# Kernel tuning notes

Measured on AMD Instinct MI355X. Metric: run time of the kernel, lower is better.

## Reference

```python
import jax, jax.numpy as jnp
import numpy as np

N_NODES = 100000   # n_nodes
N_EDGES = 1600000  # n_nodes * avg_degree(16)
D_IN = 128
D_OUT = 128


def setup_inputs() -> dict:
    key = jax.random.key(0)
    k1, k2, k3, k4, k5 = jax.random.split(key, 5)
    h = jax.random.normal(k1, (N_NODES, D_IN), dtype=jnp.float32)
    edge_src = jax.random.randint(k2, (N_EDGES,), 0, N_NODES, dtype=jnp.int32)
    edge_dst = jax.random.randint(k3, (N_EDGES,), 0, N_NODES, dtype=jnp.int32)
    # Linear params, init per reset_parameters: U(-stdv, stdv), stdv = 1/sqrt(in_feats)
    stdv = 1.0 / np.sqrt(D_IN)
    W = jax.random.uniform(k4, (D_OUT, D_IN), dtype=jnp.float32, minval=-stdv, maxval=stdv)
    b = jax.random.uniform(k5, (D_OUT,), dtype=jnp.float32, minval=-stdv, maxval=stdv)
    return {"h": h, "edge_src": edge_src, "edge_dst": edge_dst, "W": W, "b": b}


def reference(h, edge_src, edge_dst, W, b):
    # update_all(copy_src('h'), sum) == neighbor-sum aggregation (SpMM with 0/1 adjacency)
    ah = jax.ops.segment_sum(h[edge_src], edge_dst, num_segments=N_NODES)  # [N, D_IN]
    # dense linear + activation fused on the aggregated features
    return jax.nn.relu(ah @ W.T + b)  # [N, D_OUT]
```

## Files before the change

kernel.cpp:

```cpp
#include <hip/hip_runtime.h>

#define D 128
#define BKT_SHIFT 9
#define BKT_SIZE 512
#define P1_EPB 4096
#define CNT_BLOCKS 256
#define PARTIALS_INTS (256 * 256)
#define SW_LDU 68

typedef __attribute__((ext_vector_type(8))) short bf16x8;
typedef __attribute__((ext_vector_type(4))) float f32x4;

__device__ inline unsigned int pack2bf(float a, float b) {
    unsigned int ua = __float_as_uint(a);
    unsigned int ub = __float_as_uint(b);
    ua = (ua + 0x7fffu + ((ua >> 16) & 1u)) >> 16;
    ub = (ub + 0x7fffu + ((ub >> 16) & 1u)) >> 16;
    return ua | (ub << 16);
}
__device__ inline unsigned short pack1bf(float a) {
    unsigned int ua = __float_as_uint(a);
    return (unsigned short)((ua + 0x7fffu + ((ua >> 16) & 1u)) >> 16);
}


__global__ __launch_bounds__(256) void bucket_count_kernel(
    const int* __restrict__ edst, int* __restrict__ partials, int n_edges, int epb)
{
    __shared__ int hcnt[256];
    const int tid = threadIdx.x;
    hcnt[tid] = 0;
    __syncthreads();
    const int base = blockIdx.x * epb;
    const int lim = min(epb, n_edges - base);
    int k = tid;
    for (; k + 768 < lim; k += 1024) {
        int d0 = edst[base + k];
        int d1 = edst[base + k + 256];
        int d2 = edst[base + k + 512];
        int d3 = edst[base + k + 768];
        atomicAdd(&hcnt[d0 >> BKT_SHIFT], 1);
        atomicAdd(&hcnt[d1 >> BKT_SHIFT], 1);
        atomicAdd(&hcnt[d2 >> BKT_SHIFT], 1);
        atomicAdd(&hcnt[d3 >> BKT_SHIFT], 1);
    }
    for (; k < lim; k += 256)
        atomicAdd(&hcnt[edst[base + k] >> BKT_SHIFT], 1);
    __syncthreads();
    partials[(blockIdx.x << 8) + tid] = hcnt[tid];
}

__global__ __launch_bounds__(256) void bucket_scan_kernel(
    const int* __restrict__ partials, int* __restrict__ bucketBase,
    int* __restrict__ bucketCur, int nbk)
{
    __shared__ int s[256];
    const int t = threadIdx.x;
    int sum = 0;
    #pragma unroll 8
    for (int b = 0; b < CNT_BLOCKS; b++) sum += partials[(b << 8) + t];
    int v = (t < nbk) ? sum : 0;
    s[t] = v;
    __syncthreads();
    #pragma unroll
    for (int off = 1; off < 256; off <<= 1) {
        int x = (t >= off) ? s[t - off] : 0;
        __syncthreads();
        s[t] += x;
        __syncthreads();
    }
    if (t < nbk) {
        int base = s[t] - v;
        bucketBase[t] = base;
        bucketCur[t] = base;
    }
}

__global__ __launch_bounds__(256) void p1_partition_kernel(
    const int* __restrict__ esrc, const int* __restrict__ edst,
    int* __restrict__ bucketCur, unsigned int* __restrict__ pairs, int n_edges)
{
    __shared__ int hist[256];
    __shared__ int lbase[256];
    __shared__ int gbase[256];
    __shared__ int cur[256];
    __shared__ unsigned int buf[P1_EPB];
    __shared__ unsigned char bkt8[P1_EPB];
    const int tid = threadIdx.x;
    const int base = blockIdx.x * P1_EPB;
    hist[tid] = 0;
    __syncthreads();
    unsigned int pk[16]; int bk[16];
    #pragma unroll
    for (int k = 0; k < 16; k++) {
        int e = base + k * 256 + tid;
        if (e < n_edges) {
            int sv = esrc[e], dv = edst[e];
            bk[k] = dv >> BKT_SHIFT;
            pk[k] = ((unsigned)sv << BKT_SHIFT) | (unsigned)(dv & (BKT_SIZE - 1));
            atomicAdd(&hist[bk[k]], 1);
        } else bk[k] = -1;
    }
    __syncthreads();
    const int v = hist[tid];
    if (v > 0) gbase[tid] = atomicAdd(&bucketCur[tid], v);
    lbase[tid] = v;
    __syncthreads();
    #pragma unroll
    for (int off = 1; off < 256; off <<= 1) {
        int x = (tid >= off) ? lbase[tid - off] : 0;
        __syncthreads();
        lbase[tid] += x;
        __syncthreads();
    }
    const int excl = lbase[tid] - v;
    __syncthreads();
    lbase[tid] = excl;
    cur[tid] = excl;
    __syncthreads();
    #pragma unroll
    for (int k = 0; k < 16; k++) {
        if (bk[k] >= 0) {
            int loc = atomicAdd(&cur[bk[k]], 1);
            buf[loc] = pk[k];
            bkt8[loc] = (unsigned char)bk[k];
        }
    }
    __syncthreads();
    const int total = min(P1_EPB, n_edges - base);
    for (int i = tid; i < total; i += 256) {
        int b = bkt8[i];
        pairs[gbase[b] + (i - lbase[b])] = buf[i];
    }
}

__global__ __launch_bounds__(256) void p2_sort_gemm_kernel(
    const unsigned int* __restrict__ pairs, const int* __restrict__ bucketBase,
    int* __restrict__ sorted_src, int* __restrict__ gstart, int* __restrict__ gend,
    const float* __restrict__ h, const float* __restrict__ W,
    unsigned short* __restrict__ z,
    int n_nodes, int n_edges, int nbk)
{
    __shared__ union SU {
        struct { int hist[BKT_SIZE]; int cur[BKT_SIZE]; int sb[256]; } s;
        unsigned int sW[128 * SW_LDU];
    } u;
    const int tid = threadIdx.x;

    if ((int)blockIdx.x < nbk) {
        const int bkt = blockIdx.x;
        const int nbase = bkt << BKT_SHIFT;
        const int pstart = bucketBase[bkt];
        const int pend = (bkt == nbk - 1) ? n_edges : bucketBase[bkt + 1];
        u.s.hist[tid] = 0; u.s.hist[tid + 256] = 0;
        __syncthreads();
        {
            int j = pstart + tid;
            for (; j + 768 < pend; j += 1024) {
                unsigned int q0 = pairs[j];
                unsigned int q1 = pairs[j + 256];
                unsigned int q2 = pairs[j + 512];
                unsigned int q3 = pairs[j + 768];
                atomicAdd(&u.s.hist[q0 & (BKT_SIZE - 1)], 1);
                atomicAdd(&u.s.hist[q1 & (BKT_SIZE - 1)], 1);
                atomicAdd(&u.s.hist[q2 & (BKT_SIZE - 1)], 1);
                atomicAdd(&u.s.hist[q3 & (BKT_SIZE - 1)], 1);
            }
            for (; j < pend; j += 256)
                atomicAdd(&u.s.hist[pairs[j] & (BKT_SIZE - 1)], 1);
        }
        __syncthreads();
        int a  = u.s.hist[2 * tid];
        int b2 = u.s.hist[2 * tid + 1];
        int psum = a + b2;
        u.s.sb[tid] = psum;
        __syncthreads();
        #pragma unroll
        for (int off = 1; off < 256; off <<= 1) {
            int x = (tid >= off) ? u.s.sb[tid - off] : 0;
            __syncthreads();
            u.s.sb[tid] += x;
            __syncthreads();
        }
        int pexcl = u.s.sb[tid] - psum;
        u.s.cur[2 * tid] = pexcl;
        u.s.cur[2 * tid + 1] = pexcl + a;
        __syncthreads();
        for (int i = tid; i < BKT_SIZE; i += 256) {
            int nd = nbase + i;
            if (nd < n_nodes) {
                int st = pstart + u.s.cur[i];
                gstart[nd] = st;
                gend[nd] = st + u.s.hist[i];
            }
        }
        __syncthreads();
        {
            int j = pstart + tid;
            for (; j + 768 < pend; j += 1024) {
                unsigned int q0 = pairs[j];
                unsigned int q1 = pairs[j + 256];
                unsigned int q2 = pairs[j + 512];
                unsigned int q3 = pairs[j + 768];
                int p0 = pstart + atomicAdd(&u.s.cur[q0 & (BKT_SIZE - 1)], 1);
                int p1 = pstart + atomicAdd(&u.s.cur[q1 & (BKT_SIZE - 1)], 1);
                int p2 = pstart + atomicAdd(&u.s.cur[q2 & (BKT_SIZE - 1)], 1);
                int p3 = pstart + atomicAdd(&u.s.cur[q3 & (BKT_SIZE - 1)], 1);
                sorted_src[p0] = (int)(q0 >> BKT_SHIFT);
                sorted_src[p1] = (int)(q1 >> BKT_SHIFT);
                sorted_src[p2] = (int)(q2 >> BKT_SHIFT);
                sorted_src[p3] = (int)(q3 >> BKT_SHIFT);
            }
            for (; j < pend; j += 256) {
                unsigned int p = pairs[j];
                int local = p & (BKT_SIZE - 1);
                int pos = pstart + atomicAdd(&u.s.cur[local], 1);
                sorted_src[pos] = (int)(p >> BKT_SHIFT);
            }
        }
    } else {
        const int gbid = blockIdx.x - nbk;
        for (int i = tid; i < 4096; i += 256) {
            float4 w = ((const float4*)W)[i];
            int row = i >> 5, c4 = i & 31;
            unsigned int* dst = &u.sW[row * SW_LDU + c4 * 2];
            dst[0] = pack2bf(w.x, w.y);
            dst[1] = pack2bf(w.z, w.w);
        }
        __syncthreads();

        const int wave = tid >> 6;
        const int lane = tid & 63;
        const int m = lane & 15;
        const int q = lane >> 4;
        const int r0 = gbid * 64 + wave * 16;
        const int arow = r0 + m;
        const bool rvalid = arow < n_nodes;

        bf16x8 afrag[4];
        #pragma unroll
        for (int ks = 0; ks < 4; ks++) {
            float4 x = make_float4(0.f, 0.f, 0.f, 0.f), y = x;
            if (rvalid) {
                const float4* p = (const float4*)(h + (size_t)arow * D + ks * 32 + q * 8);
                x = p[0]; y = p[1];
            }
            union { unsigned int uu[4]; bf16x8 v; } cvt;
            cvt.uu[0] = pack2bf(x.x, x.y);
            cvt.uu[1] = pack2bf(x.z, x.w);
            cvt.uu[2] = pack2bf(y.x, y.y);
            cvt.uu[3] = pack2bf(y.z, y.w);
            afrag[ks] = cvt.v;
        }

        f32x4 acc[8];
        #pragma unroll
        for (int ct = 0; ct < 8; ct++) acc[ct] = (f32x4){0.f, 0.f, 0.f, 0.f};

        #pragma unroll
        for (int ct = 0; ct < 8; ct++) {
            #pragma unroll
            for (int ks = 0; ks < 4; ks++) {
                const unsigned int* p = &u.sW[(ct * 16 + m) * SW_LDU + ks * 16 + q * 4];
                union { uint4 uu; bf16x8 v; } bu;
                bu.uu = *(const uint4*)p;
                acc[ct] = __builtin_amdgcn_mfma_f32_16x16x32_bf16(afrag[ks], bu.v, acc[ct], 0, 0, 0);
            }
        }

        __syncthreads();
        unsigned short* lds_us = (unsigned short*)u.sW;
        #pragma unroll
        for (int ct = 0; ct < 8; ct++) {
            #pragma unroll
            for (int i = 0; i < 4; i++) {
                lds_us[(wave * 16 + q * 4 + i) * 130 + ct * 16 + m] = pack1bf(acc[ct][i]);
            }
        }
        __syncthreads();
        const unsigned int* lds32 = (const unsigned int*)u.sW;
        const int r0blk = gbid * 64;
        #pragma unroll
        for (int pass = 0; pass < 4; pass++) {
            int idx = pass * 256 + tid;
            int row = idx >> 4;
            int c16 = idx & 15;
            int r = r0blk + row;
            if (r < n_nodes) {
                int bo = row * 65 + c16 * 4;
                uint4 val;
                val.x = lds32[bo]; val.y = lds32[bo + 1];
                val.z = lds32[bo + 2]; val.w = lds32[bo + 3];
                ((uint4*)z)[(size_t)r * 16 + c16] = val;
            }
        }
    }
}

__global__ __launch_bounds__(256) void p2_sort_kernel(
    const unsigned int* __restrict__ pairs, const int* __restrict__ bucketBase,
    int* __restrict__ sorted_src, int* __restrict__ gstart, int* __restrict__ gend,
    int n_nodes, int n_edges, int nbk)
{
    __shared__ int hist[BKT_SIZE];
    __shared__ int cur[BKT_SIZE];
    __shared__ int sb[256];
    const int tid = threadIdx.x;
    const int bkt = blockIdx.x;
    const int nbase = bkt << BKT_SHIFT;
    const int pstart = bucketBase[bkt];
    const int pend = (bkt == nbk - 1) ? n_edges : bucketBase[bkt + 1];
    hist[tid] = 0; hist[tid + 256] = 0;
    __syncthreads();
    for (int j = pstart + tid; j < pend; j += 256)
        atomicAdd(&hist[pairs[j] & (BKT_SIZE - 1)], 1);
    __syncthreads();
    int a  = hist[2 * tid];
    int b2 = hist[2 * tid + 1];
    int psum = a + b2;
    sb[tid] = psum;
    __syncthreads();
    #pragma unroll
    for (int off = 1; off < 256; off <<= 1) {
        int x = (tid >= off) ? sb[tid - off] : 0;
        __syncthreads();
        sb[tid] += x;
        __syncthreads();
    }
    int pexcl = sb[tid] - psum;
    cur[2 * tid] = pexcl;
    cur[2 * tid + 1] = pexcl + a;
    __syncthreads();
    for (int i = tid; i < BKT_SIZE; i += 256) {
        int nd = nbase + i;
        if (nd < n_nodes) {
            int st = pstart + cur[i];
            gstart[nd] = st;
            gend[nd] = st + hist[i];
        }
    }
    __syncthreads();
    for (int j = pstart + tid; j < pend; j += 256) {
        unsigned int p = pairs[j];
        int local = p & (BKT_SIZE - 1);
        int pos = pstart + atomicAdd(&cur[local], 1);
        sorted_src[pos] = (int)(p >> BKT_SHIFT);
    }
}

__global__ __launch_bounds__(256) void gemm_z_kernel(
    const float* __restrict__ h, const float* __restrict__ W,
    unsigned short* __restrict__ z, int n_nodes)
{
    __shared__ unsigned int sW[128 * SW_LDU];
    const int tid = threadIdx.x;
    for (int i = tid; i < 4096; i += 256) {
        float4 w = ((const float4*)W)[i];
        int row = i >> 5, c4 = i & 31;
        unsigned int* dst = &sW[row * SW_LDU + c4 * 2];
        dst[0] = pack2bf(w.x, w.y);
        dst[1] = pack2bf(w.z, w.w);
    }
    __syncthreads();

    const int wave = tid >> 6;
    const int lane = tid & 63;
    const int m = lane & 15;
    const int q = lane >> 4;
    const int r0 = blockIdx.x * 64 + wave * 16;
    const int arow = r0 + m;
    const bool rvalid = arow < n_nodes;

    bf16x8 afrag[4];
    #pragma unroll
    for (int ks = 0; ks < 4; ks++) {
        float4 x = make_float4(0.f, 0.f, 0.f, 0.f), y = x;
        if (rvalid) {
            const float4* p = (const float4*)(h + (size_t)arow * D + ks * 32 + q * 8);
            x = p[0]; y = p[1];
        }
        union { unsigned int u[4]; bf16x8 v; } cvt;
        cvt.u[0] = pack2bf(x.x, x.y);
        cvt.u[1] = pack2bf(x.z, x.w);
        cvt.u[2] = pack2bf(y.x, y.y);
        cvt.u[3] = pack2bf(y.z, y.w);
        afrag[ks] = cvt.v;
    }

    f32x4 acc[8];
    #pragma unroll
    for (int ct = 0; ct < 8; ct++) acc[ct] = (f32x4){0.f, 0.f, 0.f, 0.f};

    #pragma unroll
    for (int ct = 0; ct < 8; ct++) {
        #pragma unroll
        for (int ks = 0; ks < 4; ks++) {
            const unsigned int* p = &sW[(ct * 16 + m) * SW_LDU + ks * 16 + q * 4];
            union { uint4 u; bf16x8 v; } bu;
            bu.u = *(const uint4*)p;
            acc[ct] = __builtin_amdgcn_mfma_f32_16x16x32_bf16(afrag[ks], bu.v, acc[ct], 0, 0, 0);
        }
    }

    __syncthreads();
    unsigned short* lds_us = (unsigned short*)sW;
    #pragma unroll
    for (int ct = 0; ct < 8; ct++) {
        #pragma unroll
        for (int i = 0; i < 4; i++) {
            lds_us[(wave * 16 + q * 4 + i) * 130 + ct * 16 + m] = pack1bf(acc[ct][i]);
        }
    }
    __syncthreads();
    const unsigned int* lds32 = (const unsigned int*)sW;
    const int r0blk = blockIdx.x * 64;
    #pragma unroll
    for (int pass = 0; pass < 4; pass++) {
        int idx = pass * 256 + tid;
        int row = idx >> 4;
        int c16 = idx & 15;
        int r = r0blk + row;
        if (r < n_nodes) {
            int bo = row * 65 + c16 * 4;
            uint4 val;
            val.x = lds32[bo]; val.y = lds32[bo + 1];
            val.z = lds32[bo + 2]; val.w = lds32[bo + 3];
            ((uint4*)z)[(size_t)r * 16 + c16] = val;
        }
    }
}

__global__ __launch_bounds__(256) void gather_row_kernel(
    const unsigned short* __restrict__ z, const int* __restrict__ gstart,
    const int* __restrict__ gend, const int* __restrict__ sorted_src,
    const float* __restrict__ b, float* __restrict__ out, int n_nodes,
    int node_base)
{
    const int tid = threadIdx.x;
    const int node = node_base + blockIdx.x * 16 + (tid >> 4);
    const int lane = tid & 15;
    if (node >= n_nodes) return;
    int e = gstart[node];
    const int end = gend[node];
    const uint4* __restrict__ z4 = (const uint4*)z;
    float acc[8];
    #pragma unroll
    for (int i = 0; i < 8; i++) acc[i] = 0.f;
#define ADDV(v) do { \
    acc[0] += __uint_as_float((v).x << 16); acc[1] += __uint_as_float((v).x & 0xffff0000u); \
    acc[2] += __uint_as_float((v).y << 16); acc[3] += __uint_as_float((v).y & 0xffff0000u); \
    acc[4] += __uint_as_float((v).z << 16); acc[5] += __uint_as_float((v).z & 0xffff0000u); \
    acc[6] += __uint_as_float((v).w << 16); acc[7] += __uint_as_float((v).w & 0xffff0000u); } while (0)
    for (; e + 4 <= end; e += 4) {
        int s0 = sorted_src[e + 0];
        int s1 = sorted_src[e + 1];
        int s2 = sorted_src[e + 2];
        int s3 = sorted_src[e + 3];
        uint4 v0 = z4[(size_t)s0 * 16 + lane];
        uint4 v1 = z4[(size_t)s1 * 16 + lane];
        uint4 v2 = z4[(size_t)s2 * 16 + lane];
        uint4 v3 = z4[(size_t)s3 * 16 + lane];
        ADDV(v0); ADDV(v1); ADDV(v2); ADDV(v3);
    }
    for (; e < end; e++) {
        uint4 v = z4[(size_t)sorted_src[e] * 16 + lane];
        ADDV(v);
    }
#undef ADDV
    float4 b0 = ((const float4*)b)[lane * 2];
    float4 b1 = ((const float4*)b)[lane * 2 + 1];
    float4* o = (float4*)(out + (size_t)node * D + lane * 8);
    o[0] = make_float4(fmaxf(acc[0] + b0.x, 0.f), fmaxf(acc[1] + b0.y, 0.f),
                       fmaxf(acc[2] + b0.z, 0.f), fmaxf(acc[3] + b0.w, 0.f));
    o[1] = make_float4(fmaxf(acc[4] + b1.x, 0.f), fmaxf(acc[5] + b1.y, 0.f),
                       fmaxf(acc[6] + b1.z, 0.f), fmaxf(acc[7] + b1.w, 0.f));
}


__global__ __launch_bounds__(256) void hist_kernel(
    const int* __restrict__ edst, int* __restrict__ cnt, int n_edges)
{
    int gid = blockIdx.x * 256 + threadIdx.x;
    if (gid < n_edges) atomicAdd(&cnt[edst[gid]], 1);
}

__global__ __launch_bounds__(256) void scanA_kernel(
    const int* __restrict__ cnt, int* __restrict__ localoff,
    int* __restrict__ blocksums, int n)
{
    __shared__ int s[256];
    const int t = threadIdx.x;
    const int base = blockIdx.x * 1024 + t * 4;
    int v[4]; int sum = 0;
    #pragma unroll
    for (int i = 0; i < 4; i++) {
        int idx = base + i;
        v[i] = (idx < n) ? cnt[idx] : 0;
        sum += v[i];
    }
    s[t] = sum;
    __syncthreads();
    #pragma unroll
    for (int off = 1; off < 256; off <<= 1) {
        int x = (t >= off) ? s[t - off] : 0;
        __syncthreads();
        s[t] += x;
        __syncthreads();
    }
    int excl = s[t] - sum;
    int run = 0;
    #pragma unroll
    for (int i = 0; i < 4; i++) {
        int idx = base + i;
        if (idx < n) localoff[idx] = excl + run;
        run += v[i];
    }
    if (t == 255) blocksums[blockIdx.x] = s[255];
}

__global__ __launch_bounds__(256) void scanB_kernel(
    const int* __restrict__ blocksums, int* __restrict__ blockoffs, int nb)
{
    __shared__ int s[256];
    const int t = threadIdx.x;
    int v = (t < nb) ? blocksums[t] : 0;
    s[t] = v;
    __syncthreads();
    #pragma unroll
    for (int off = 1; off < 256; off <<= 1) {
        int x = (t >= off) ? s[t - off] : 0;
        __syncthreads();
        s[t] += x;
        __syncthreads();
    }
    if (t < nb) blockoffs[t] = s[t] - v;
}

__global__ __launch_bounds__(256) void scanC_kernel(
    const int* __restrict__ localoff, const int* __restrict__ blockoffs,
    int* __restrict__ outoffs, int* __restrict__ cursor, int n)
{
    int gid = blockIdx.x * 256 + threadIdx.x;
    if (gid >= n) return;
    int v = localoff[gid] + blockoffs[blockIdx.x >> 2];
    outoffs[gid] = v;
    if (cursor) cursor[gid] = v;
}

__global__ __launch_bounds__(256) void place_kernel(
    const int* __restrict__ esrc, const int* __restrict__ edst,
    int* __restrict__ cursor, int* __restrict__ sorted_src, int n_edges)
{
    int gid = blockIdx.x * 256 + threadIdx.x;
    if (gid >= n_edges) return;
    int d = edst[gid];
    int pos = atomicAdd(&cursor[d], 1);
    sorted_src[pos] = esrc[gid];
}

__global__ __launch_bounds__(256) void gather_kernel(
    const float* __restrict__ h, const int* __restrict__ offs,
    const int* __restrict__ endp, const int* __restrict__ sorted_src,
    float* __restrict__ out, int n_nodes)
{
    const int tid = threadIdx.x;
    const int node = blockIdx.x * 8 + (tid >> 5);
    const int lane = tid & 31;
    if (node >= n_nodes) return;
    const int start = offs[node];
    const int end = endp[node];
    const float4* __restrict__ h4 = (const float4*)h;
    float4 acc = make_float4(0.f, 0.f, 0.f, 0.f);
    for (int e = start; e < end; e++) {
        float4 a = h4[(size_t)sorted_src[e] * 32 + lane];
        acc.x += a.x; acc.y += a.y; acc.z += a.z; acc.w += a.w;
    }
    ((float4*)out)[(size_t)node * 32 + lane] = acc;
}

__global__ __launch_bounds__(256) void scatter_kernel(
    const float* __restrict__ h, const int* __restrict__ esrc,
    const int* __restrict__ edst, float* __restrict__ out, int n_edges)
{
    int gid = blockIdx.x * 256 + threadIdx.x;
    int e = gid >> 5;
    int l = gid & 31;
    if (e >= n_edges) return;
    int s = esrc[e];
    int d = edst[e];
    float4 v = ((const float4*)(h + (size_t)s * D))[l];
    float* o = out + (size_t)d * D + (size_t)l * 4;
    atomicAdd(o + 0, v.x);
    atomicAdd(o + 1, v.y);
    atomicAdd(o + 2, v.z);
    atomicAdd(o + 3, v.w);
}

__global__ __launch_bounds__(256) void mfma_gemm_relu_kernel(
    float* __restrict__ io, const float* __restrict__ W,
    const float* __restrict__ b, int n_nodes)
{
    __shared__ unsigned int sW[128 * SW_LDU];
    const int tid = threadIdx.x;
    for (int i = tid; i < 4096; i += 256) {
        float4 w = ((const float4*)W)[i];
        int row = i >> 5, c4 = i & 31;
        unsigned int* dst = &sW[row * SW_LDU + c4 * 2];
        dst[0] = pack2bf(w.x, w.y);
        dst[1] = pack2bf(w.z, w.w);
    }
    __syncthreads();
    const int wave = tid >> 6;
    const int lane = tid & 63;
    const int m = lane & 15;
    const int q = lane >> 4;
    const int r0 = blockIdx.x * 64 + wave * 16;
    const int arow = r0 + m;
    const bool rvalid = arow < n_nodes;
    bf16x8 afrag[4];
    #pragma unroll
    for (int ks = 0; ks < 4; ks++) {
        float4 x = make_float4(0.f, 0.f, 0.f, 0.f), y = x;
        if (rvalid) {
            const float4* p = (const float4*)(io + (size_t)arow * D + ks * 32 + q * 8);
            x = p[0]; y = p[1];
        }
        union { unsigned int u[4]; bf16x8 v; } cvt;
        cvt.u[0] = pack2bf(x.x, x.y);
        cvt.u[1] = pack2bf(x.z, x.w);
        cvt.u[2] = pack2bf(y.x, y.y);
        cvt.u[3] = pack2bf(y.z, y.w);
        afrag[ks] = cvt.v;
    }
    f32x4 acc[8];
    #pragma unroll
    for (int ct = 0; ct < 8; ct++) acc[ct] = (f32x4){0.f, 0.f, 0.f, 0.f};
    #pragma unroll
    for (int ct = 0; ct < 8; ct++) {
        #pragma unroll
        for (int ks = 0; ks < 4; ks++) {
            const unsigned int* p = &sW[(ct * 16 + m) * SW_LDU + ks * 16 + q * 4];
            union { uint4 u; bf16x8 v; } bu;
            bu.u = *(const uint4*)p;
            acc[ct] = __builtin_amdgcn_mfma_f32_16x16x32_bf16(afrag[ks], bu.v, acc[ct], 0, 0, 0);
        }
    }
    #pragma unroll
    for (int ct = 0; ct < 8; ct++) {
        int col = ct * 16 + m;
        float bias = b[col];
        #pragma unroll
        for (int i = 0; i < 4; i++) {
            int r = r0 + q * 4 + i;
            if (r < n_nodes) {
                float v = acc[ct][i] + bias;
                io[(size_t)r * D + col] = v > 0.f ? v : 0.f;
            }
        }
    }
}

extern "C" void kernel_launch(void* const* d_in, const int* in_sizes, int n_in,
                              void* d_out, int out_size, void* d_ws, size_t ws_size,
                              hipStream_t stream) {
    const float* h    = (const float*)d_in[0];
    const int*   esrc = (const int*)d_in[1];
    const int*   edst = (const int*)d_in[2];
    const float* W    = (const float*)d_in[3];
    const float* b    = (const float*)d_in[4];
    float* out = (float*)d_out;
    const int n_nodes = in_sizes[0] / D;
    const int n_edges = in_sizes[1];
    const int NB  = (n_nodes + 1023) / 1024;
    const int NBK = (n_nodes + BKT_SIZE - 1) / BKT_SIZE;

    size_t fixed = ((size_t)2 * n_nodes + PARTIALS_INTS + 2 * NBK + (size_t)n_edges) * 4;
    size_t pairs_off = (fixed + 15) & ~(size_t)15;
    size_t z_off = (pairs_off + (size_t)n_edges * 4 + 15) & ~(size_t)15;
    size_t need_fused = z_off + (size_t)n_nodes * D * 2;

    size_t zone_bytes = (size_t)n_edges * 4;
    size_t zb2 = (size_t)n_nodes * D * 2;
    if (zb2 > zone_bytes) zone_bytes = zb2;
    size_t need_main = pairs_off + zone_bytes;

    const int cnt_epb = (n_edges + CNT_BLOCKS - 1) / CNT_BLOCKS;

    if (ws_size >= need_fused && NBK <= 256 && n_nodes <= (1 << 22)) {
        int* gstart     = (int*)d_ws;
        int* gend       = gstart + n_nodes;
        int* partials   = gend + n_nodes;
        int* bucketBase = partials + PARTIALS_INTS;
        int* bucketCur  = bucketBase + NBK;
        int* sorted_src = bucketCur + NBK;
        unsigned int* pairs = (unsigned int*)((char*)d_ws + pairs_off);
        unsigned short* z   = (unsigned short*)((char*)d_ws + z_off);

        bucket_count_kernel<<<CNT_BLOCKS, 256, 0, stream>>>(
            edst, partials, n_edges, cnt_epb);
        bucket_scan_kernel<<<1, 256, 0, stream>>>(partials, bucketBase, bucketCur, NBK);
        p1_partition_kernel<<<(n_edges + P1_EPB - 1) / P1_EPB, 256, 0, stream>>>(
            esrc, edst, bucketCur, pairs, n_edges);
        const int gemmBlocks = (n_nodes + 63) / 64;
        p2_sort_gemm_kernel<<<NBK + gemmBlocks, 256, 0, stream>>>(
            pairs, bucketBase, sorted_src, gstart, gend, h, W, z,
            n_nodes, n_edges, NBK);
        gather_row_kernel<<<(n_nodes + 15) / 16, 256, 0, stream>>>(
            z, gstart, gend, sorted_src, b, out, n_nodes, 0);
        return;
    }

    if (ws_size >= need_main && NBK <= 256 && n_nodes <= (1 << 23)) {
        int* gstart     = (int*)d_ws;
        int* gend       = gstart + n_nodes;
        int* partials   = gend + n_nodes;
        int* bucketBase = partials + PARTIALS_INTS;
        int* bucketCur  = bucketBase + NBK;
        int* sorted_src = bucketCur + NBK;
        void* zone = (char*)d_ws + pairs_off;
        unsigned int* pairs = (unsigned int*)zone;
        unsigned short* z = (unsigned short*)zone;

        bucket_count_kernel<<<CNT_BLOCKS, 256, 0, stream>>>(
            edst, partials, n_edges, cnt_epb);
        bucket_scan_kernel<<<1, 256, 0, stream>>>(partials, bucketBase, bucketCur, NBK);
        p1_partition_kernel<<<(n_edges + P1_EPB - 1) / P1_EPB, 256, 0, stream>>>(
            esrc, edst, bucketCur, pairs, n_edges);
        p2_sort_kernel<<<NBK, 256, 0, stream>>>(
            pairs, bucketBase, sorted_src, gstart, gend, n_nodes, n_edges, NBK);
        gemm_z_kernel<<<(n_nodes + 63) / 64, 256, 0, stream>>>(h, W, z, n_nodes);
        gather_row_kernel<<<(n_nodes + 15) / 16, 256, 0, stream>>>(
            z, gstart, gend, sorted_src, b, out, n_nodes, 0);
        return;
    }

    size_t csr_ints = (size_t)3 * n_nodes + 2 * NB + (size_t)n_edges;
    size_t needB = csr_ints * sizeof(int);
    if (ws_size >= needB && NB <= 256) {
        int* cnt        = (int*)d_ws;
        int* offs       = cnt + n_nodes;
        int* cursor     = offs + n_nodes;
        int* blocksums  = cursor + n_nodes;
        int* blockoffs  = blocksums + NB;
        int* sorted_src = blockoffs + NB;

        hipMemsetAsync(cnt, 0, (size_t)n_nodes * sizeof(int), stream);
        hist_kernel<<<(n_edges + 255) / 256, 256, 0, stream>>>(edst, cnt, n_edges);
        scanA_kernel<<<NB, 256, 0, stream>>>(cnt, offs, blocksums, n_nodes);
        scanB_kernel<<<1, 256, 0, stream>>>(blocksums, blockoffs, NB);
        scanC_kernel<<<(n_nodes + 255) / 256, 256, 0, stream>>>(
            offs, blockoffs, cnt, cursor, n_nodes);
        place_kernel<<<(n_edges + 255) / 256, 256, 0, stream>>>(
            esrc, edst, cursor, sorted_src, n_edges);
        gather_kernel<<<(n_nodes + 7) / 8, 256, 0, stream>>>(
            h, cnt, cursor, sorted_src, out, n_nodes);
    } else {
        hipMemsetAsync(out, 0, (size_t)n_nodes * D * sizeof(float), stream);
        long long total = (long long)n_edges * 32;
        scatter_kernel<<<(int)((total + 255) / 256), 256, 0, stream>>>(h, esrc, edst, out, n_edges);
    }
    mfma_gemm_relu_kernel<<<(n_nodes + 63) / 64, 256, 0, stream>>>(out, W, b, n_nodes);
}
```

Before: 236.2 us.

## Stage per-bucket sort in LDS, widen count grid, split gather launches

```diff
diff --git a/kernel.cpp b/kernel.cpp
--- a/kernel.cpp
+++ b/kernel.cpp
@@ -4,8 +4,9 @@
 #define BKT_SHIFT 9
 #define BKT_SIZE 512
 #define P1_EPB 4096
-#define CNT_BLOCKS 256
-#define PARTIALS_INTS (256 * 256)
+#define CNT_BLOCKS 512
+#define PARTIALS_INTS (512 * 256)
+#define SORT_CAP 9216
 #define SW_LDU 68
 
 typedef __attribute__((ext_vector_type(8))) short bf16x8;
@@ -142,7 +143,7 @@
     int n_nodes, int n_edges, int nbk)
 {
     __shared__ union SU {
-        struct { int hist[BKT_SIZE]; int cur[BKT_SIZE]; int sb[256]; } s;
+        struct { int hist[BKT_SIZE]; int cur[BKT_SIZE]; int sb[256]; int lbuf[SORT_CAP]; } s;
         unsigned int sW[128 * SW_LDU];
     } u;
     const int tid = threadIdx.x;
@@ -152,6 +153,7 @@
         const int nbase = bkt << BKT_SHIFT;
         const int pstart = bucketBase[bkt];
         const int pend = (bkt == nbk - 1) ? n_edges : bucketBase[bkt + 1];
+        const int cnt = pend - pstart;
         u.s.hist[tid] = 0; u.s.hist[tid + 256] = 0;
         __syncthreads();
         {
@@ -195,23 +197,34 @@
             }
         }
         __syncthreads();
-        {
-            int j = pstart + tid;
-            for (; j + 768 < pend; j += 1024) {
-                unsigned int q0 = pairs[j];
-                unsigned int q1 = pairs[j + 256];
-                unsigned int q2 = pairs[j + 512];
-                unsigned int q3 = pairs[j + 768];
-                int p0 = pstart + atomicAdd(&u.s.cur[q0 & (BKT_SIZE - 1)], 1);
-                int p1 = pstart + atomicAdd(&u.s.cur[q1 & (BKT_SIZE - 1)], 1);
-                int p2 = pstart + atomicAdd(&u.s.cur[q2 & (BKT_SIZE - 1)], 1);
-                int p3 = pstart + atomicAdd(&u.s.cur[q3 & (BKT_SIZE - 1)], 1);
-                sorted_src[p0] = (int)(q0 >> BKT_SHIFT);
-                sorted_src[p1] = (int)(q1 >> BKT_SHIFT);
-                sorted_src[p2] = (int)(q2 >> BKT_SHIFT);
-                sorted_src[p3] = (int)(q3 >> BKT_SHIFT);
-            }
-            for (; j < pend; j += 256) {
+        if (cnt <= SORT_CAP) {
+            {
+                int j = pstart + tid;
+                for (; j + 768 < pend; j += 1024) {
+                    unsigned int q0 = pairs[j];
+                    unsigned int q1 = pairs[j + 256];
+                    unsigned int q2 = pairs[j + 512];
+                    unsigned int q3 = pairs[j + 768];
+                    int p0 = atomicAdd(&u.s.cur[q0 & (BKT_SIZE - 1)], 1);
+                    int p1 = atomicAdd(&u.s.cur[q1 & (BKT_SIZE - 1)], 1);
+                    int p2 = atomicAdd(&u.s.cur[q2 & (BKT_SIZE - 1)], 1);
+                    int p3 = atomicAdd(&u.s.cur[q3 & (BKT_SIZE - 1)], 1);
+                    u.s.lbuf[p0] = (int)(q0 >> BKT_SHIFT);
+                    u.s.lbuf[p1] = (int)(q1 >> BKT_SHIFT);
+                    u.s.lbuf[p2] = (int)(q2 >> BKT_SHIFT);
+                    u.s.lbuf[p3] = (int)(q3 >> BKT_SHIFT);
+                }
+                for (; j < pend; j += 256) {
+                    unsigned int p = pairs[j];
+                    int pos = atomicAdd(&u.s.cur[p & (BKT_SIZE - 1)], 1);
+                    u.s.lbuf[pos] = (int)(p >> BKT_SHIFT);
+                }
+            }
+            __syncthreads();
+            for (int i = tid; i < cnt; i += 256)
+                sorted_src[pstart + i] = u.s.lbuf[i];
+        } else {
+            for (int j = pstart + tid; j < pend; j += 256) {
                 unsigned int p = pairs[j];
                 int local = p & (BKT_SIZE - 1);
                 int pos = pstart + atomicAdd(&u.s.cur[local], 1);
@@ -433,13 +446,13 @@
 __global__ __launch_bounds__(256) void gather_row_kernel(
     const unsigned short* __restrict__ z, const int* __restrict__ gstart,
     const int* __restrict__ gend, const int* __restrict__ sorted_src,
-    const float* __restrict__ b, float* __restrict__ out, int n_nodes,
+    const float* __restrict__ b, float* __restrict__ out, int n_limit,
     int node_base)
 {
     const int tid = threadIdx.x;
     const int node = node_base + blockIdx.x * 16 + (tid >> 4);
     const int lane = tid & 15;
-    if (node >= n_nodes) return;
+    if (node >= n_limit) return;
     int e = gstart[node];
     const int end = gend[node];
     const uint4* __restrict__ z4 = (const uint4*)z;
@@ -705,8 +718,14 @@
         p2_sort_gemm_kernel<<<NBK + gemmBlocks, 256, 0, stream>>>(
             pairs, bucketBase, sorted_src, gstart, gend, h, W, z,
             n_nodes, n_edges, NBK);
-        gather_row_kernel<<<(n_nodes + 15) / 16, 256, 0, stream>>>(
-            z, gstart, gend, sorted_src, b, out, n_nodes, 0);
+        const int qa = (((n_nodes + 3) / 4) + 15) & ~15;
+        int s = 0;
+        while (s < n_nodes) {
+            int e2 = min(s + qa, n_nodes);
+            gather_row_kernel<<<(e2 - s + 15) / 16, 256, 0, stream>>>(
+                z, gstart, gend, sorted_src, b, out, e2, s);
+            s = e2;
+        }
         return;
     }
 
```

Result: slower. 258.5 us (+9.4%).
